# Kernel tuning notes

Measured on AMD Instinct MI355X. Metric: run time of the kernel, lower is better.

## Reference

```python
import jax, jax.numpy as jnp
import numpy as np

B, S, D_IN, D_OUT = 4, 2048, 1024, 1024


def setup_inputs() -> dict:
    key = jax.random.key(0)
    ks = jax.random.split(key, 7)
    return {
        "X": jax.random.normal(ks[0], (B, S, D_IN), dtype=jnp.float32),
        "Wq": jax.random.normal(ks[1], (D_IN, D_OUT), dtype=jnp.float32) * (1.0 / np.sqrt(D_IN)),
        "bq": jax.random.normal(ks[2], (D_OUT,), dtype=jnp.float32) * 0.02,
        "Wk": jax.random.normal(ks[3], (D_IN, D_OUT), dtype=jnp.float32) * (1.0 / np.sqrt(D_IN)),
        "bk": jax.random.normal(ks[4], (D_OUT,), dtype=jnp.float32) * 0.02,
        "Wv": jax.random.normal(ks[5], (D_IN, D_OUT), dtype=jnp.float32) * (1.0 / np.sqrt(D_IN)),
        "bv": jax.random.normal(ks[6], (D_OUT,), dtype=jnp.float32) * 0.02,
    }


def reference(X, Wq, bq, Wk, bk, Wv, bv):
    # Linear projections (torch Linear: x @ W^T + b; here W stored as [in,out])
    Q = X @ Wq + bq  # [B,S,D]
    K = X @ Wk + bk
    V = X @ Wv + bv
    dk = jnp.sqrt(jnp.asarray(D_OUT, dtype=X.dtype))
    # Raw scores, lower-triangular ZEROING (not -inf), scale, softmax over keys.
    S_ = jnp.einsum('bqd,bkd->bqk', Q, K)
    S_ = jnp.tril(S_) / dk
    A = jax.nn.softmax(S_, axis=2)  # [B,S,S]
    # Faithful to torch.einsum('ijk,ijl->ijl', A, V): reduces A over k, scales V.
    out = jnp.einsum('bqk,bql->bql', A, V)
    return out
```

## Files before the change

### kernel.cpp

```cpp
#include <hip/hip_runtime.h>
#include <hip/hip_bf16.h>

#define DIN  1024
#define DOUT 1024
#define MROWS 8192

#define BM 128
#define BN 128
#define BK 32
#define KTILES (DIN / BK)

typedef __attribute__((ext_vector_type(8))) short short8;
typedef __attribute__((ext_vector_type(4))) float f32x4;

__device__ __forceinline__ ushort f2bf(float f) {
    union { float f; unsigned u; } x; x.f = f;
    unsigned u = x.u + 0x7fffu + ((x.u >> 16) & 1u);
    return (ushort)(u >> 16);
}

__global__ void cvt_x_kernel(const float* __restrict__ X, ushort* __restrict__ Xb, int n4) {
    int i = blockIdx.x * blockDim.x + threadIdx.x;
    int stride = gridDim.x * blockDim.x;
    const float4* X4 = (const float4*)X;
    ushort4* O4 = (ushort4*)Xb;
    for (int idx = i; idx < n4; idx += stride) {
        float4 v = X4[idx];
        ushort4 o;
        o.x = f2bf(v.x); o.y = f2bf(v.y); o.z = f2bf(v.z); o.w = f2bf(v.w);
        O4[idx] = o;
    }
}

__global__ void cvt_wt_kernel(const float* __restrict__ W, ushort* __restrict__ Wt) {
    __shared__ float tile[32][33];
    int bx = blockIdx.x * 32;
    int by = blockIdx.y * 32;
    int tx = threadIdx.x;
    int ty = threadIdx.y;
#pragma unroll
    for (int i = 0; i < 32; i += 8)
        tile[ty + i][tx] = W[(size_t)(by + ty + i) * DOUT + (bx + tx)];
    __syncthreads();
#pragma unroll
    for (int i = 0; i < 32; i += 8)
        Wt[(size_t)(bx + ty + i) * DIN + (by + tx)] = f2bf(tile[tx][ty + i]);
}

__global__ __launch_bounds__(256, 2) void gemm_bias(
    const ushort* __restrict__ Xb,
    const ushort* __restrict__ Wt,
    const float* __restrict__ bias,
    float* __restrict__ out)
{
    __shared__ ushort As[2][BM * BK];
    __shared__ ushort Bs[2][BN * BK];

    const int tid  = threadIdx.x;
    const int lane = tid & 63;
    const int wid  = tid >> 6;
    const int wr   = wid >> 1;
    const int wc   = wid & 1;

    const int bid = blockIdx.x;
    const int swz = (bid & 7) * 64 + (bid >> 3);
    const int bm = (swz >> 3) * BM;
    const int bn = (swz & 7) * BN;

    auto stageA = [&](ushort* dst, int kt) {
        const int k0 = kt * BK;
#pragma unroll
        for (int j = 0; j < 2; ++j) {
            const int cb = (wid * 2 + j) * 64;
            const int chunk = cb + lane;
            const int row = chunk >> 2;
            const int col = (chunk & 3) * 8;
            __builtin_amdgcn_global_load_lds(
                (const __attribute__((address_space(1))) void*)(Xb + (size_t)(bm + row) * DIN + k0 + col),
                (__attribute__((address_space(3))) void*)(dst + cb * 8),
                16, 0, 0);
        }
    };
    auto stageB = [&](ushort* dst, int kt) {
        const int k0 = kt * BK;
#pragma unroll
        for (int j = 0; j < 2; ++j) {
            const int cb = (wid * 2 + j) * 64;
            const int chunk = cb + lane;
            const int row = chunk >> 2;
            const int col = (chunk & 3) * 8;
            __builtin_amdgcn_global_load_lds(
                (const __attribute__((address_space(1))) void*)(Wt + (size_t)(bn + row) * DIN + k0 + col),
                (__attribute__((address_space(3))) void*)(dst + cb * 8),
                16, 0, 0);
        }
    };

    f32x4 acc[4][4];
#pragma unroll
    for (int i = 0; i < 4; ++i)
#pragma unroll
        for (int j = 0; j < 4; ++j)
            acc[i][j] = (f32x4){0.f, 0.f, 0.f, 0.f};

    auto compute = [&](const ushort* A_, const ushort* B_) {
        const int kgrp = (lane >> 4) * 8;
        short8 af[4], bf[4];
#pragma unroll
        for (int i = 0; i < 4; ++i) {
            const int ar = wr * 64 + i * 16 + (lane & 15);
            af[i] = *(const short8*)(A_ + ar * BK + kgrp);
            const int br = wc * 64 + i * 16 + (lane & 15);
            bf[i] = *(const short8*)(B_ + br * BK + kgrp);
        }
#pragma unroll
        for (int i = 0; i < 4; ++i)
#pragma unroll
            for (int j = 0; j < 4; ++j)
                acc[i][j] = __builtin_amdgcn_mfma_f32_16x16x32_bf16(af[i], bf[j], acc[i][j], 0, 0, 0);
    };

    stageA(As[0], 0);
    stageB(Bs[0], 0);
    __syncthreads();

    int cur = 0;
    for (int kt = 0; kt < KTILES - 1; ++kt) {
        stageA(As[cur ^ 1], kt + 1);
        stageB(Bs[cur ^ 1], kt + 1);
        compute(As[cur], Bs[cur]);
        __syncthreads();
        cur ^= 1;
    }
    compute(As[cur], Bs[cur]);

    const int crow = bm + wr * 64;
    const int ccol = bn + wc * 64;
#pragma unroll
    for (int j = 0; j < 4; ++j) {
        const int col = ccol + j * 16 + (lane & 15);
        const float bval = bias[col];
#pragma unroll
        for (int i = 0; i < 4; ++i) {
            const int row0 = crow + i * 16 + (lane >> 4) * 4;
#pragma unroll
            for (int r = 0; r < 4; ++r)
                out[(size_t)(row0 + r) * DOUT + col] = acc[i][j][r] + bval;
        }
    }
}

__global__ void gemm_naive(const float* __restrict__ X, const float* __restrict__ W,
                           const float* __restrict__ b, float* __restrict__ out) {
    int n = blockIdx.x * blockDim.x + threadIdx.x;
    int m = blockIdx.y;
    float acc = b[n];
    for (int k = 0; k < DIN; ++k)
        acc += X[(size_t)m * DIN + k] * W[(size_t)k * DOUT + n];
    out[(size_t)m * DOUT + n] = acc;
}

extern "C" void kernel_launch(void* const* d_in, const int* in_sizes, int n_in,
                              void* d_out, int out_size, void* d_ws, size_t ws_size,
                              hipStream_t stream) {
    const float* X  = (const float*)d_in[0];
    const float* Wv = (const float*)d_in[5];
    const float* bv = (const float*)d_in[6];
    float* out = (float*)d_out;

    const size_t xb_elems = (size_t)MROWS * DIN;
    const size_t wt_elems = (size_t)DOUT * DIN;
    const size_t needed = (xb_elems + wt_elems) * sizeof(ushort);

    if (ws_size < needed) {
        dim3 g(DOUT / 256, MROWS);
        gemm_naive<<<g, 256, 0, stream>>>(X, Wv, bv, out);
        return;
    }

    ushort* Xb = (ushort*)d_ws;
    ushort* Wt = Xb + xb_elems;

    cvt_x_kernel<<<2048, 256, 0, stream>>>(X, Xb, (int)(xb_elems / 4));
    cvt_wt_kernel<<<dim3(DOUT / 32, DIN / 32), dim3(32, 8), 0, stream>>>(Wv, Wt);
    gemm_bias<<<512, 256, 0, stream>>>(Xb, Wt, bv, out);
}
```

Before: 44.65 us.

## Enlarge GEMM tiles and triple-buffer LDS with swizzled, half-stage pipelining

Grows the bf16 MFMA GEMM block tile to 256x128 with a K step of 64 and 512 threads, so the grid becomes 256 blocks. LDS becomes a three-deep ring buffer with an XOR-swizzled column layout to avoid bank conflicts. Each K tile is split into two phases that interleave async global-to-LDS staging with MFMA work, using explicit vmcnt waits, barriers and s_setprio. The aim is to hide load latency and raise arithmetic intensity, at the cost of much more LDS per block (about 147KB), which limits each CU to one block and leaves a single wave of blocks across the device.

```diff
diff --git a/kernel.cpp b/kernel.cpp
--- a/kernel.cpp
+++ b/kernel.cpp
@@ -5,10 +5,10 @@
 #define DOUT 1024
 #define MROWS 8192
 
-#define BM 128
+#define BM 256
 #define BN 128
-#define BK 32
-#define KTILES (DIN / BK)
+#define BK 64
+#define NKT (DIN / BK)
 
 typedef __attribute__((ext_vector_type(8))) short short8;
 typedef __attribute__((ext_vector_type(4))) float f32x4;
@@ -47,14 +47,14 @@
         Wt[(size_t)(bx + ty + i) * DIN + (by + tx)] = f2bf(tile[tx][ty + i]);
 }
 
-__global__ __launch_bounds__(256, 2) void gemm_bias(
+__global__ __launch_bounds__(512, 2) void gemm_bias(
     const ushort* __restrict__ Xb,
     const ushort* __restrict__ Wt,
     const float* __restrict__ bias,
     float* __restrict__ out)
 {
-    __shared__ ushort As[2][BM * BK];
-    __shared__ ushort Bs[2][BN * BK];
+    __shared__ ushort As[3][BM * BK];
+    __shared__ ushort Bs[3][BN * BK];
 
     const int tid  = threadIdx.x;
     const int lane = tid & 63;
@@ -63,35 +63,28 @@
     const int wc   = wid & 1;
 
     const int bid = blockIdx.x;
-    const int swz = (bid & 7) * 64 + (bid >> 3);
+    const int swz = (bid & 7) * 32 + (bid >> 3);
     const int bm = (swz >> 3) * BM;
     const int bn = (swz & 7) * BN;
 
-    auto stageA = [&](ushort* dst, int kt) {
-        const int k0 = kt * BK;
+    auto stageHalf = [&](int b, int kt, int h) {
 #pragma unroll
         for (int j = 0; j < 2; ++j) {
-            const int cb = (wid * 2 + j) * 64;
-            const int chunk = cb + lane;
-            const int row = chunk >> 2;
-            const int col = (chunk & 3) * 8;
+            const int c   = j * 512 + tid;
+            const int rl  = c >> 3;
+            const int scc = (c & 7) ^ (rl & 7);
             __builtin_amdgcn_global_load_lds(
-                (const __attribute__((address_space(1))) void*)(Xb + (size_t)(bm + row) * DIN + k0 + col),
-                (__attribute__((address_space(3))) void*)(dst + cb * 8),
+                (const __attribute__((address_space(1))) void*)(Xb + (size_t)(bm + h * 128 + rl) * DIN + kt * BK + scc * 8),
+                (__attribute__((address_space(3))) void*)(&As[b][h * 8192 + (j * 512 + wid * 64) * 8]),
                 16, 0, 0);
         }
-    };
-    auto stageB = [&](ushort* dst, int kt) {
-        const int k0 = kt * BK;
-#pragma unroll
-        for (int j = 0; j < 2; ++j) {
-            const int cb = (wid * 2 + j) * 64;
-            const int chunk = cb + lane;
-            const int row = chunk >> 2;
-            const int col = (chunk & 3) * 8;
+        {
+            const int c   = tid;
+            const int rl  = c >> 3;
+            const int scc = (c & 7) ^ (rl & 7);
             __builtin_amdgcn_global_load_lds(
-                (const __attribute__((address_space(1))) void*)(Wt + (size_t)(bn + row) * DIN + k0 + col),
-                (__attribute__((address_space(3))) void*)(dst + cb * 8),
+                (const __attribute__((address_space(1))) void*)(Wt + (size_t)(bn + h * 64 + rl) * DIN + kt * BK + scc * 8),
+                (__attribute__((address_space(3))) void*)(&Bs[b][h * 4096 + wid * 512]),
                 16, 0, 0);
         }
     };
@@ -103,49 +96,63 @@
         for (int j = 0; j < 4; ++j)
             acc[i][j] = (f32x4){0.f, 0.f, 0.f, 0.f};
 
-    auto compute = [&](const ushort* A_, const ushort* B_) {
-        const int kgrp = (lane >> 4) * 8;
-        short8 af[4], bf[4];
+    auto phase = [&](int buf, int ks, bool doStage, int sbuf, int skt, int sh,
+                     int wait, bool endBar) {
+        short8 af[4], bfr[4];
+        const int sc = ((ks * 4 + (lane >> 4)) ^ (lane & 7)) * 8;
+        const int am = wr * 64 + (lane & 15);
+        const int bnr = wc * 64 + (lane & 15);
 #pragma unroll
-        for (int i = 0; i < 4; ++i) {
-            const int ar = wr * 64 + i * 16 + (lane & 15);
-            af[i] = *(const short8*)(A_ + ar * BK + kgrp);
-            const int br = wc * 64 + i * 16 + (lane & 15);
-            bf[i] = *(const short8*)(B_ + br * BK + kgrp);
-        }
+        for (int i = 0; i < 4; ++i)
+            af[i] = *(const short8*)(&As[buf][(am + i * 16) * 64 + sc]);
+#pragma unroll
+        for (int j = 0; j < 4; ++j)
+            bfr[j] = *(const short8*)(&Bs[buf][(bnr + j * 16) * 64 + sc]);
+        if (doStage) stageHalf(sbuf, skt, sh);
+        __builtin_amdgcn_s_barrier();
+        asm volatile("s_waitcnt lgkmcnt(0)" ::: "memory");
+        __builtin_amdgcn_sched_barrier(0);
+        __builtin_amdgcn_s_setprio(1);
 #pragma unroll
         for (int i = 0; i < 4; ++i)
 #pragma unroll
             for (int j = 0; j < 4; ++j)
-                acc[i][j] = __builtin_amdgcn_mfma_f32_16x16x32_bf16(af[i], bf[j], acc[i][j], 0, 0, 0);
+                acc[i][j] = __builtin_amdgcn_mfma_f32_16x16x32_bf16(af[i], bfr[j], acc[i][j], 0, 0, 0);
+        __builtin_amdgcn_s_setprio(0);
+        if (wait == 2)      asm volatile("s_waitcnt vmcnt(6)" ::: "memory");
+        else if (wait == 1) asm volatile("s_waitcnt vmcnt(0)" ::: "memory");
+        if (endBar) __builtin_amdgcn_s_barrier();
     };
 
-    stageA(As[0], 0);
-    stageB(Bs[0], 0);
-    __syncthreads();
+    stageHalf(0, 0, 0);
+    stageHalf(0, 0, 1);
+    stageHalf(1, 1, 0);
+    stageHalf(1, 1, 1);
+    asm volatile("s_waitcnt vmcnt(6)" ::: "memory");
+    __builtin_amdgcn_s_barrier();
 
-    int cur = 0;
-    for (int kt = 0; kt < KTILES - 1; ++kt) {
-        stageA(As[cur ^ 1], kt + 1);
-        stageB(Bs[cur ^ 1], kt + 1);
-        compute(As[cur], Bs[cur]);
-        __syncthreads();
-        cur ^= 1;
+    for (int t = 0; t < NKT - 2; ++t) {
+        const int buf  = t % 3;
+        const int sbuf = (t + 2) % 3;
+        phase(buf, 0, true, sbuf, t + 2, 0, 0, true);
+        phase(buf, 1, true, sbuf, t + 2, 1, 2, true);
     }
-    compute(As[cur], Bs[cur]);
+    phase((NKT - 2) % 3, 0, false, 0, 0, 0, 0, true);
+    phase((NKT - 2) % 3, 1, false, 0, 0, 0, 1, true);
+    phase((NKT - 1) % 3, 0, false, 0, 0, 0, 0, true);
+    phase((NKT - 1) % 3, 1, false, 0, 0, 0, 0, false);
 
-    const int crow = bm + wr * 64;
-    const int ccol = bn + wc * 64;
+    const int crow = bm + wr * 64 + (lane >> 4) * 4;
+    const int ccol = bn + wc * 64 + (lane & 15);
 #pragma unroll
     for (int j = 0; j < 4; ++j) {
-        const int col = ccol + j * 16 + (lane & 15);
+        const int col = ccol + j * 16;
         const float bval = bias[col];
 #pragma unroll
         for (int i = 0; i < 4; ++i) {
-            const int row0 = crow + i * 16 + (lane >> 4) * 4;
 #pragma unroll
             for (int r = 0; r < 4; ++r)
-                out[(size_t)(row0 + r) * DOUT + col] = acc[i][j][r] + bval;
+                out[(size_t)(crow + i * 16 + r) * DOUT + col] = acc[i][j][r] + bval;
         }
     }
 }
@@ -183,5 +190,5 @@
 
     cvt_x_kernel<<<2048, 256, 0, stream>>>(X, Xb, (int)(xb_elems / 4));
     cvt_wt_kernel<<<dim3(DOUT / 32, DIN / 32), dim3(32, 8), 0, stream>>>(Wv, Wt);
-    gemm_bias<<<512, 256, 0, stream>>>(Xb, Wt, bv, out);
+    gemm_bias<<<256, 512, 0, stream>>>(Xb, Wt, bv, out);
 }
```

After: 39.05 us. -12.6%, faster.
